# Optimization experiments

Measured on AMD Instinct MI355X. Metric: run time of the kernel, lower is better.

## Reference

```python
import jax, jax.numpy as jnp
import numpy as np

MIN_POS = 1e-6
EPS = 1e-20
B, S, F_IN, E, H = 2, 1024, 768, 768, 12
DH = E // H   # nnmf in_features per head (64)
FH = E // H   # nnmf out_features per head (hidden_features=embed_dim default)
N_NNMF_ITERS = 3
N_ALPHA_ITERS = 3


def l1norm(x, axis=-1):
    # F.normalize(x, p=1, dim=axis, eps=1e-20) for non-negative x
    return x / jnp.maximum(jnp.sum(jnp.abs(x), axis=axis, keepdims=True), EPS)


def setup_inputs() -> dict:
    key = jax.random.key(0)
    k = jax.random.split(key, 6)
    return {
        "x": jax.random.normal(k[0], (B, S, F_IN), jnp.float32),
        "embed_w": jax.random.normal(k[1], (E, F_IN), jnp.float32) * 0.02,
        "embed_b": jnp.zeros((E,), jnp.float32),
        "nnmf_w": jax.random.uniform(k[2], (FH, DH), jnp.float32),  # non-negative NMF dictionary
        "out_w": jax.random.normal(k[3], (F_IN, E), jnp.float32) * 0.02,
        "out_b": jnp.zeros((F_IN,), jnp.float32),
    }


def reference(x, embed_w, embed_b, nnmf_w, out_w, out_b):
    # normalize NMF weight rows (p=1 over in_features), as nnmf_layer.normalize_weights
    W = nnmf_w / jnp.maximum(jnp.sum(nnmf_w, axis=1, keepdims=True), EPS)  # [FH, DH]

    # embed + clamp positive, split heads
    xe = jnp.clip(x @ embed_w.T + embed_b, MIN_POS)            # [B,S,E]
    xe = xe.reshape(B, S, H, DH)                                # [B,S,H,DH]

    # NNMFDense: prepared_input = l1-normalized input (normalize_input_dim=-1)
    inp = l1norm(xe)                                            # [B,S,H,DH]
    h = l1norm(jnp.ones((B, S, H, FH), x.dtype))                # init hidden
    rec = inp
    for _ in range(N_NNMF_ITERS):
        rec = l1norm(jnp.clip(h @ W, MIN_POS))                  # reconstruction [B,S,H,DH]
        h = l1norm(jnp.clip(h * ((inp / rec) @ W.T), MIN_POS))  # multiplicative update

    # normalize_h (p=1, dim=-1)
    h = l1norm(h)                                               # [B,S,H,FH] -> 'bohf'

    # alpha dynamics fixed point
    alpha = jnp.ones((B, H, S, S), x.dtype)                     # 'bhoi'
    h_rec_input = rec * inp                                     # [B,S,H,DH]
    for _ in range(N_ALPHA_ITERS):
        h_mixed = jnp.einsum('bohf,bhoi->bihf', h, alpha)       # [B,S,H,FH]
        arec_inv = 1.0 / (h_mixed @ W + EPS)                    # _reconstruct -> [B,S,H,DH]
        alpha = alpha * jnp.einsum('bohf,bihf->bhoi', h_rec_input, arec_inv)

    out = jnp.einsum('bohf,bhoi->bihf', h, alpha)               # [B,S,H,FH]
    out = out.reshape(B, S, E)                                  # flatten heads
    return out @ out_w.T + out_b                                # out_project
```

## Files before the change

kernel.cpp:

```cpp
#include <hip/hip_runtime.h>

#define B_  2
#define S_  1024
#define FIN 768
#define E_  768
#define H_  12
#define DH  64

typedef unsigned int uint;
typedef unsigned short ushort;
typedef __attribute__((ext_vector_type(8))) short short8;
typedef __attribute__((ext_vector_type(4))) float floatx4;

__device__ __forceinline__ ushort f2bf(float f) {
    uint u = __float_as_uint(f);
    return (ushort)((u + 0x7fffu + ((u >> 16) & 1u)) >> 16);
}

__device__ __forceinline__ uint4 pack8(const ushort* p) {
    uint4 r;
    r.x = (uint)p[0] | ((uint)p[1] << 16);
    r.y = (uint)p[2] | ((uint)p[3] << 16);
    r.z = (uint)p[4] | ((uint)p[5] << 16);
    r.w = (uint)p[6] | ((uint)p[7] << 16);
    return r;
}

__device__ __forceinline__ void split8v(float4 a, float4 b, short8& hi, short8& lo) {
    float v[8] = {a.x, a.y, a.z, a.w, b.x, b.y, b.z, b.w};
    ushort h[8], l[8];
#pragma unroll
    for (int j = 0; j < 8; ++j) {
        h[j] = f2bf(v[j]);
        l[j] = f2bf(v[j] - __uint_as_float(((uint)h[j]) << 16));
    }
    uint4 H = pack8(h), L = pack8(l);
    hi = *(short8*)&H;
    lo = *(short8*)&L;
}

__global__ __launch_bounds__(256) void k_conv(const float* __restrict__ xs,
                                              const float* __restrict__ ew,
                                              const float* __restrict__ nw,
                                              ushort* __restrict__ xsH,
                                              ushort* __restrict__ xsL,
                                              ushort* __restrict__ ewH,
                                              ushort* __restrict__ ewL,
                                              float* __restrict__ Wn,
                                              float* __restrict__ r1inv,
                                              ushort* __restrict__ Wfrag) {
    __shared__ float Wl[64 * 65];
    const int tid = threadIdx.x, bid = blockIdx.x;

    if (bid < 768) {
        const size_t i = ((size_t)bid * 256 + tid) * 8;
        short8 hi, lo;
        split8v(*(const float4*)(xs + i), *(const float4*)(xs + i + 4), hi, lo);
        *(short8*)(xsH + i) = hi;
        *(short8*)(xsL + i) = lo;
        return;
    }
    if (bid < 1056) {
        const size_t i = ((size_t)(bid - 768) * 256 + tid) * 8;
        short8 hi, lo;
        split8v(*(const float4*)(ew + i), *(const float4*)(ew + i + 4), hi, lo);
        *(short8*)(ewH + i) = hi;
        *(short8*)(ewL + i) = lo;
        return;
    }

    const int f = tid >> 2, q = tid & 3;
    float v[16];
    float s = 0.f;
#pragma unroll
    for (int i = 0; i < 16; ++i) { v[i] = nw[f * 64 + q * 16 + i]; s += v[i]; }
    s += __shfl_xor(s, 1, 64);
    s += __shfl_xor(s, 2, 64);
    const float inv = 1.f / fmaxf(s, 1e-20f);
    float w[16];
#pragma unroll
    for (int i = 0; i < 16; ++i) {
        w[i] = v[i] * inv;
        Wn[f * 64 + q * 16 + i] = w[i];
        Wl[f * 65 + q * 16 + i] = w[i];
    }
    __syncthreads();
    if (tid < 64) {
        float cs = 0.f;
        for (int ff = 0; ff < 64; ++ff) cs += Wl[ff * 65 + tid];
        float t = fmaxf(cs * (1.f / 64.f), 1e-6f);
        float S = t;
#pragma unroll
        for (int m = 1; m < 64; m <<= 1) S += __shfl_xor(S, m, 64);
        S = fmaxf(S, 1e-20f);
        r1inv[tid] = S / t;
    }
    {
        short8 h0, l0, h1, l1;
        split8v(make_float4(w[0], w[1], w[2], w[3]),
                make_float4(w[4], w[5], w[6], w[7]), h0, l0);
        split8v(make_float4(w[8], w[9], w[10], w[11]),
                make_float4(w[12], w[13], w[14], w[15]), h1, l1);
        ushort* WwH = Wfrag + 2 * 4096;
        ushort* WwL = Wfrag + 3 * 4096;
        *(short8*)(WwH + f * 64 + q * 16) = h0;
        *(short8*)(WwH + f * 64 + q * 16 + 8) = h1;
        *(short8*)(WwL + f * 64 + q * 16) = l0;
        *(short8*)(WwL + f * 64 + q * 16 + 8) = l1;
    }
    {
        float t[16];
#pragma unroll
        for (int i = 0; i < 16; ++i) t[i] = Wl[(q * 16 + i) * 65 + f];
        short8 h0, l0, h1, l1;
        split8v(make_float4(t[0], t[1], t[2], t[3]),
                make_float4(t[4], t[5], t[6], t[7]), h0, l0);
        split8v(make_float4(t[8], t[9], t[10], t[11]),
                make_float4(t[12], t[13], t[14], t[15]), h1, l1);
        ushort* WtH = Wfrag;
        ushort* WtL = Wfrag + 4096;
        *(short8*)(WtH + f * 64 + q * 16) = h0;
        *(short8*)(WtH + f * 64 + q * 16 + 8) = h1;
        *(short8*)(WtL + f * 64 + q * 16) = l0;
        *(short8*)(WtL + f * 64 + q * 16 + 8) = l1;
    }
}

__device__ __forceinline__ void mfma_matvec(const float srcC[4][4], float* T,
                                            int lm, int lq,
                                            const ushort* WH, const ushort* WL,
                                            floatx4 out[4]) {
    __builtin_amdgcn_wave_barrier();
#pragma unroll
    for (int nt = 0; nt < 4; ++nt)
#pragma unroll
        for (int r = 0; r < 4; ++r)
            T[(lq * 4 + r) * 68 + nt * 16 + lm] = srcC[nt][r];
    __builtin_amdgcn_wave_barrier();
    float4 a00 = *(const float4*)&T[lm * 68 + lq * 8];
    float4 a01 = *(const float4*)&T[lm * 68 + lq * 8 + 4];
    float4 a10 = *(const float4*)&T[lm * 68 + 32 + lq * 8];
    float4 a11 = *(const float4*)&T[lm * 68 + 32 + lq * 8 + 4];
    __builtin_amdgcn_wave_barrier();
    short8 A0h, A0l, A1h, A1l;
    split8v(a00, a01, A0h, A0l);
    split8v(a10, a11, A1h, A1l);
#pragma unroll
    for (int nt = 0; nt < 4; ++nt) {
        const int row = (nt * 16 + lm) * 72;
        short8 b0h = *(const short8*)&WH[row + lq * 8];
        short8 b0l = *(const short8*)&WL[row + lq * 8];
        short8 b1h = *(const short8*)&WH[row + 32 + lq * 8];
        short8 b1l = *(const short8*)&WL[row + 32 + lq * 8];
        floatx4 acc0 = (floatx4)0.f, acc1 = (floatx4)0.f;
        acc0 = __builtin_amdgcn_mfma_f32_16x16x32_bf16(A0h, b0h, acc0, 0, 0, 0);
        acc0 = __builtin_amdgcn_mfma_f32_16x16x32_bf16(A0l, b0h, acc0, 0, 0, 0);
        acc0 = __builtin_amdgcn_mfma_f32_16x16x32_bf16(A0h, b0l, acc0, 0, 0, 0);
        acc1 = __builtin_amdgcn_mfma_f32_16x16x32_bf16(A1h, b1h, acc1, 0, 0, 0);
        acc1 = __builtin_amdgcn_mfma_f32_16x16x32_bf16(A1l, b1h, acc1, 0, 0, 0);
        acc1 = __builtin_amdgcn_mfma_f32_16x16x32_bf16(A1h, b1l, acc1, 0, 0, 0);
        out[nt] = acc0 + acc1;
    }
}

__global__ __launch_bounds__(256) void k_embed_nnmf(const ushort* __restrict__ xsH,
                                                    const ushort* __restrict__ xsL,
                                                    const ushort* __restrict__ ewH,
                                                    const ushort* __restrict__ ewL,
                                                    const float* __restrict__ eb,
                                                    const ushort* __restrict__ Wfrag,
                                                    const float* __restrict__ r1inv,
                                                    float* __restrict__ hout,
                                                    float* __restrict__ hriout,
                                                    float* __restrict__ mp0) {
    __shared__ __align__(16) unsigned char smem[73728];
    ushort* const sm = (ushort*)smem;
    const int tid = threadIdx.x;
    const int bid = blockIdx.x;

    const int head = bid % 12;
    const int tok0 = (bid / 12) * 64;

    const int wv = tid >> 6, lane = tid & 63;
    const int mbase = wv * 16;
    const int lm = lane & 15, lq = lane >> 4;

    floatx4 accA[4], accB[4];
#pragma unroll
    for (int nt = 0; nt < 4; ++nt) { accA[nt] = (floatx4)0.f; accB[nt] = (floatx4)0.f; }

    const int srow = tid >> 2, skq = (tid & 3) * 16;
    const int off = srow * 72 + skq;
    const ushort* xh = xsH + (size_t)(tok0 + srow) * FIN + skq;
    const ushort* xl = xsL + (size_t)(tok0 + srow) * FIN + skq;
    const ushort* wh = ewH + (size_t)(head * 64 + srow) * FIN + skq;
    const ushort* wl = ewL + (size_t)(head * 64 + srow) * FIN + skq;

    short8 pa[4], pb[4];
    pa[0] = *(const short8*)(xh);  pa[1] = *(const short8*)(xh + 8);
    pa[2] = *(const short8*)(xl);  pa[3] = *(const short8*)(xl + 8);
    pb[0] = *(const short8*)(wh);  pb[1] = *(const short8*)(wh + 8);
    pb[2] = *(const short8*)(wl);  pb[3] = *(const short8*)(wl + 8);
    {
        ushort* b0 = sm;
        *(short8*)&b0[off]            = pa[0];
        *(short8*)&b0[off + 8]        = pa[1];
        *(short8*)&b0[4608 + off]     = pa[2];
        *(short8*)&b0[4608 + off + 8] = pa[3];
        *(short8*)&b0[9216 + off]     = pb[0];
        *(short8*)&b0[9216 + off + 8] = pb[1];
        *(short8*)&b0[13824 + off]    = pb[2];
        *(short8*)&b0[13824 + off + 8]= pb[3];
    }
    pa[0] = *(const short8*)(xh + 64);  pa[1] = *(const short8*)(xh + 72);
    pa[2] = *(const short8*)(xl + 64);  pa[3] = *(const short8*)(xl + 72);
    pb[0] = *(const short8*)(wh + 64);  pb[1] = *(const short8*)(wh + 72);
    pb[2] = *(const short8*)(wl + 64);  pb[3] = *(const short8*)(wl + 72);
    __syncthreads();

#pragma unroll 2
    for (int kb = 0; kb < 12; ++kb) {
        const int cur = kb & 1;
        const ushort* cb = sm + cur * 18432;
#pragma unroll
        for (int ch = 0; ch < 2; ++ch) {
            const int ko = ch * 32 + lq * 8;
            short8 ah = *(const short8*)&cb[(mbase + lm) * 72 + ko];
            short8 al = *(const short8*)&cb[4608 + (mbase + lm) * 72 + ko];
#pragma unroll
            for (int nt = 0; nt < 4; ++nt) {
                short8 bh = *(const short8*)&cb[9216 + (nt * 16 + lm) * 72 + ko];
                short8 bl = *(const short8*)&cb[13824 + (nt * 16 + lm) * 72 + ko];
                accA[nt] = __builtin_amdgcn_mfma_f32_16x16x32_bf16(ah, bh, accA[nt], 0, 0, 0);
                accB[nt] = __builtin_amdgcn_mfma_f32_16x16x32_bf16(al, bh, accB[nt], 0, 0, 0);
                accB[nt] = __builtin_amdgcn_mfma_f32_16x16x32_bf16(ah, bl, accB[nt], 0, 0, 0);
            }
        }
        if (kb + 1 < 12) {
            ushort* sb = sm + (cur ^ 1) * 18432;
            *(short8*)&sb[off]            = pa[0];
            *(short8*)&sb[off + 8]        = pa[1];
            *(short8*)&sb[4608 + off]     = pa[2];
            *(short8*)&sb[4608 + off + 8] = pa[3];
            *(short8*)&sb[9216 + off]     = pb[0];
            *(short8*)&sb[9216 + off + 8] = pb[1];
            *(short8*)&sb[13824 + off]    = pb[2];
            *(short8*)&sb[13824 + off + 8]= pb[3];
        }
        if (kb + 2 < 12) {
            const int ko = (kb + 2) * 64;
            pa[0] = *(const short8*)(xh + ko);  pa[1] = *(const short8*)(xh + ko + 8);
            pa[2] = *(const short8*)(xl + ko);  pa[3] = *(const short8*)(xl + ko + 8);
            pb[0] = *(const short8*)(wh + ko);  pb[1] = *(const short8*)(wh + ko + 8);
            pb[2] = *(const short8*)(wl + ko);  pb[3] = *(const short8*)(wl + ko + 8);
        }
        __syncthreads();
    }

    const int wrow = tid >> 2, wkq = (tid & 3) * 16;
    const int wg = wrow * 64 + wkq;
    short8 wt0 = *(const short8*)(Wfrag + wg);
    short8 wt1 = *(const short8*)(Wfrag + wg + 8);
    short8 wt2 = *(const short8*)(Wfrag + 4096 + wg);
    short8 wt3 = *(const short8*)(Wfrag + 4096 + wg + 8);
    short8 ww0 = *(const short8*)(Wfrag + 8192 + wg);
    short8 ww1 = *(const short8*)(Wfrag + 8192 + wg + 8);
    short8 ww2 = *(const short8*)(Wfrag + 12288 + wg);
    short8 ww3 = *(const short8*)(Wfrag + 12288 + wg + 8);
    float r1c[4];
#pragma unroll
    for (int nt = 0; nt < 4; ++nt) r1c[nt] = r1inv[nt * 16 + lm];

    float inpC[4][4];
    {
        float bb[4];
#pragma unroll
        for (int nt = 0; nt < 4; ++nt) bb[nt] = eb[head * 64 + nt * 16 + lm];
#pragma unroll
        for (int r = 0; r < 4; ++r) {
            float e[4];
            float p = 0.f;
#pragma unroll
            for (int nt = 0; nt < 4; ++nt) {
                e[nt] = fmaxf((accA[nt][r] + accB[nt][r]) + bb[nt], 1e-6f);
                p += e[nt];
            }
            p += __shfl_xor(p, 1, 64);
            p += __shfl_xor(p, 2, 64);
            p += __shfl_xor(p, 4, 64);
            p += __shfl_xor(p, 8, 64);
            const float inv = 1.f / fmaxf(p, 1e-20f);
#pragma unroll
            for (int nt = 0; nt < 4; ++nt) inpC[nt][r] = e[nt] * inv;
        }
    }

    __syncthreads();
    ushort* WtH = sm;
    ushort* WtL = sm + 4608;
    ushort* WwH = sm + 9216;
    ushort* WwL = sm + 13824;
    float*  Tb  = (float*)(smem + 36864);
    float*  pbuf= (float*)(smem + 54272);
    float*  T   = Tb + wv * (16 * 68);
    {
        const int l = wrow * 72 + wkq;
        *(short8*)&WtH[l]     = wt0;
        *(short8*)&WtH[l + 8] = wt1;
        *(short8*)&WtL[l]     = wt2;
        *(short8*)&WtL[l + 8] = wt3;
        *(short8*)&WwH[l]     = ww0;
        *(short8*)&WwH[l + 8] = ww1;
        *(short8*)&WwL[l]     = ww2;
        *(short8*)&WwL[l + 8] = ww3;
    }
    __syncthreads();

    const size_t obase = ((size_t)((tok0 >> 10) * 12 + head) * 1024 + (tok0 & 1023));
    const size_t rowbase = obase + wv * 16;

    float hC[4][4], recC[4][4];
    {
        float qC[4][4];
#pragma unroll
        for (int nt = 0; nt < 4; ++nt)
#pragma unroll
            for (int r = 0; r < 4; ++r) qC[nt][r] = inpC[nt][r] * r1c[nt];
        floatx4 u[4];
        mfma_matvec(qC, T, lm, lq, WwH, WwL, u);
#pragma unroll
        for (int nt = 0; nt < 4; ++nt)
#pragma unroll
            for (int r = 0; r < 4; ++r)
                hC[nt][r] = fmaxf(u[nt][r] * (1.f / 64.f), 1e-6f);
#pragma unroll
        for (int r = 0; r < 4; ++r) {
            float s = (hC[0][r] + hC[1][r]) + (hC[2][r] + hC[3][r]);
            s += __shfl_xor(s, 1, 64); s += __shfl_xor(s, 2, 64);
            s += __shfl_xor(s, 4, 64); s += __shfl_xor(s, 8, 64);
            const float inv = __builtin_amdgcn_rcpf(fmaxf(s, 1e-20f));
#pragma unroll
            for (int nt = 0; nt < 4; ++nt) hC[nt][r] *= inv;
        }
    }
#pragma unroll 1
    for (int it = 0; it < 2; ++it) {
        floatx4 t[4];
        mfma_matvec(hC, T, lm, lq, WtH, WtL, t);
        float tC[4][4], qC[4][4];
#pragma unroll
        for (int nt = 0; nt < 4; ++nt)
#pragma unroll
            for (int r = 0; r < 4; ++r) tC[nt][r] = fmaxf(t[nt][r], 1e-6f);
#pragma unroll
        for (int r = 0; r < 4; ++r) {
            float s = (tC[0][r] + tC[1][r]) + (tC[2][r] + tC[3][r]);
            s += __shfl_xor(s, 1, 64); s += __shfl_xor(s, 2, 64);
            s += __shfl_xor(s, 4, 64); s += __shfl_xor(s, 8, 64);
            s = fmaxf(s, 1e-20f);
            const float invS = __builtin_amdgcn_rcpf(s);
#pragma unroll
            for (int nt = 0; nt < 4; ++nt) {
                recC[nt][r] = tC[nt][r] * invS;
                qC[nt][r] = inpC[nt][r] * s * __builtin_amdgcn_rcpf(tC[nt][r]);
            }
        }
        floatx4 u[4];
        mfma_matvec(qC, T, lm, lq, WwH, WwL, u);
#pragma unroll
        for (int nt = 0; nt < 4; ++nt)
#pragma unroll
            for (int r = 0; r < 4; ++r)
                hC[nt][r] = fmaxf(hC[nt][r] * u[nt][r], 1e-6f);
#pragma unroll
        for (int r = 0; r < 4; ++r) {
            float s = (hC[0][r] + hC[1][r]) + (hC[2][r] + hC[3][r]);
            s += __shfl_xor(s, 1, 64); s += __shfl_xor(s, 2, 64);
            s += __shfl_xor(s, 4, 64); s += __shfl_xor(s, 8, 64);
            const float inv = __builtin_amdgcn_rcpf(fmaxf(s, 1e-20f));
#pragma unroll
            for (int nt = 0; nt < 4; ++nt) hC[nt][r] *= inv;
        }
    }
#pragma unroll
    for (int r = 0; r < 4; ++r) {
        float s = (hC[0][r] + hC[1][r]) + (hC[2][r] + hC[3][r]);
        s += __shfl_xor(s, 1, 64); s += __shfl_xor(s, 2, 64);
        s += __shfl_xor(s, 4, 64); s += __shfl_xor(s, 8, 64);
        const float inv = __builtin_amdgcn_rcpf(fmaxf(s, 1e-20f));
#pragma unroll
        for (int nt = 0; nt < 4; ++nt) hC[nt][r] *= inv;
    }

#pragma unroll
    for (int nt = 0; nt < 4; ++nt)
#pragma unroll
        for (int r = 0; r < 4; ++r) {
            const size_t o = (rowbase + lq * 4 + r) * 64 + nt * 16 + lm;
            hout[o] = hC[nt][r];
            hriout[o] = recC[nt][r] * inpC[nt][r];
        }

    float hs[4];
#pragma unroll
    for (int nt = 0; nt < 4; ++nt) {
        float s = (hC[nt][0] + hC[nt][1]) + (hC[nt][2] + hC[nt][3]);
        s += __shfl_xor(s, 16, 64);
        s += __shfl_xor(s, 32, 64);
        hs[nt] = s;
    }
    pbuf[wv * 64 + lq * 16 + lm] = hs[lq];
    __syncthreads();
    if (tid < 64) {
        float tot = (pbuf[tid] + pbuf[64 + tid]) + (pbuf[128 + tid] + pbuf[192 + tid]);
        mp0[(obase >> 6) * 64 + tid] = tot;
    }
}

__global__ __launch_bounds__(256) void k_alpha_step(const float* __restrict__ hin,
                                                    const float* __restrict__ hri,
                                                    const float* __restrict__ Wn,
                                                    const float* __restrict__ mp_in,
                                                    float* __restrict__ mp_out,
                                                    float* __restrict__ c,
                                                    int it) {
    __shared__ float mred[4][64];
    __shared__ float mv[64];
    __shared__ float vv[64];
    __shared__ float cl[64];
    const int tid = threadIdx.x;
    const int bh = blockIdx.x >> 4;
    const int chunk = blockIdx.x & 15;
    const size_t rowbase = (size_t)bh * 1024 + chunk * 64;

    {
        int f = tid & 63, p = tid >> 6;
        float s = 0.f;
#pragma unroll
        for (int pp = 0; pp < 4; ++pp)
            s += mp_in[((size_t)bh * 16 + p * 4 + pp) * 64 + f];
        mred[p][f] = s;
    }
    __syncthreads();
    if (tid < 64)
        mv[tid] = (mred[0][tid] + mred[1][tid]) + (mred[2][tid] + mred[3][tid]);
    __syncthreads();
    {
        int d = tid & 63, qq = tid >> 6;
        float r = 0.f;
#pragma unroll
        for (int ff = 0; ff < 16; ++ff)
            r = fmaf(mv[qq * 16 + ff], Wn[(size_t)(qq * 16 + ff) * 64 + d], r);
        mred[qq][d] = r;
    }
    __syncthreads();
    if (tid < 64)
        vv[tid] = 1.f / (((mred[0][tid] + mred[1][tid]) + (mred[2][tid] + mred[3][tid])) + 1e-20f);
    __syncthreads();
    {
        int o = tid >> 2, dq = tid & 3;
        const float* rp = hri + (rowbase + o) * 64 + dq * 16;
        float dot = 0.f;
#pragma unroll
        for (int t4 = 0; t4 < 16; t4 += 4) {
            float4 r4 = *(const float4*)(rp + t4);
            dot = fmaf(r4.x, vv[dq * 16 + t4 + 0], dot);
            dot = fmaf(r4.y, vv[dq * 16 + t4 + 1], dot);
            dot = fmaf(r4.z, vv[dq * 16 + t4 + 2], dot);
            dot = fmaf(r4.w, vv[dq * 16 + t4 + 3], dot);
        }
        dot += __shfl_xor(dot, 1, 64);
        dot += __shfl_xor(dot, 2, 64);
        float cn = dot;
        if (it >= 2) cn *= c[rowbase + o];
        if (dq == 0) { c[rowbase + o] = cn; cl[o] = cn; }
    }
    __syncthreads();
    {
        const int f4 = (tid & 15) * 4, ogr = tid >> 4;
        float4 a = make_float4(0.f, 0.f, 0.f, 0.f);
#pragma unroll
        for (int oi = 0; oi < 4; ++oi) {
            int o = ogr * 4 + oi;
            float4 h4 = *(const float4*)(hin + (rowbase + o) * 64 + f4);
            float cv = cl[o];
            a.x = fmaf(h4.x, cv, a.x); a.y = fmaf(h4.y, cv, a.y);
            a.z = fmaf(h4.z, cv, a.z); a.w = fmaf(h4.w, cv, a.w);
        }
        a.x += __shfl_xor(a.x, 16, 64); a.y += __shfl_xor(a.y, 16, 64);
        a.z += __shfl_xor(a.z, 16, 64); a.w += __shfl_xor(a.w, 16, 64);
        a.x += __shfl_xor(a.x, 32, 64); a.y += __shfl_xor(a.y, 32, 64);
        a.z += __shfl_xor(a.z, 32, 64); a.w += __shfl_xor(a.w, 32, 64);
        const int w = tid >> 6;
        if ((tid & 63) < 16) *(float4*)&mred[w][(tid & 15) * 4] = a;
    }
    __syncthreads();
    if (tid < 64) {
        float s = (mred[0][tid] + mred[1][tid]) + (mred[2][tid] + mred[3][tid]);
        mp_out[((size_t)bh * 16 + chunk) * 64 + tid] = s;
    }
}

__global__ __launch_bounds__(256) void k_projbcast(const float* __restrict__ mp3,
                                                   const float* __restrict__ ow,
                                                   const float* __restrict__ ob,
                                                   float* __restrict__ out) {
    __shared__ float Ml[768];
    __shared__ float ps[4][64];
    __shared__ float yseg[64];
    const int tid = threadIdx.x;
    const int b = blockIdx.x / 192;
    const int rem = blockIdx.x - b * 192;
    const int jt = rem >> 4, rg = rem & 15;
    for (int i = tid; i < 768; i += 256) {
        const int hh = i >> 6, f = i & 63;
        const float* src = mp3 + ((size_t)(b * 12 + hh) * 16) * 64 + f;
        float s = 0.f;
#pragma unroll
        for (int cc = 0; cc < 16; ++cc) s += src[cc * 64];
        Ml[i] = s;
    }
    __syncthreads();
    const int jj = tid & 63, part = tid >> 6;
    const int j = jt * 64 + jj;
    const float* row = ow + (size_t)j * 768 + part * 192;
    float acc = 0.f;
    for (int t = 0; t < 192; t += 4) {
        float4 w4 = *(const float4*)(row + t);
        acc = fmaf(w4.x, Ml[part * 192 + t + 0], acc);
        acc = fmaf(w4.y, Ml[part * 192 + t + 1], acc);
        acc = fmaf(w4.z, Ml[part * 192 + t + 2], acc);
        acc = fmaf(w4.w, Ml[part * 192 + t + 3], acc);
    }
    ps[part][jj] = acc;
    __syncthreads();
    if (tid < 64)
        yseg[tid] = ps[0][tid] + ps[1][tid] + ps[2][tid] + ps[3][tid] + ob[jt * 64 + tid];
    __syncthreads();
    const int r0 = tid >> 2, c4 = (tid & 3) * 16;
    float4 v4[4];
#pragma unroll
    for (int q = 0; q < 4; ++q) v4[q] = *(const float4*)&yseg[c4 + q * 4];
    float* dst = out + ((size_t)(b * 1024 + rg * 64 + r0)) * 768 + jt * 64 + c4;
#pragma unroll
    for (int q = 0; q < 4; ++q) *(float4*)(dst + q * 4) = v4[q];
}

extern "C" void kernel_launch(void* const* d_in, const int* in_sizes, int n_in,
                              void* d_out, int out_size, void* d_ws, size_t ws_size,
                              hipStream_t stream) {
    const float* xs = (const float*)d_in[0];
    const float* ew = (const float*)d_in[1];
    const float* eb = (const float*)d_in[2];
    const float* nw = (const float*)d_in[3];
    const float* ow = (const float*)d_in[4];
    const float* ob = (const float*)d_in[5];
    float* out = (float*)d_out;

    float* ws    = (float*)d_ws;
    float* h     = ws + 1572864;
    float* hri   = ws + 3145728;
    float* Wn    = ws + 4718592;
    float* r1inv = ws + 4722688;
    float* mp0   = ws + 4722944;
    float* mp1   = ws + 4747520;
    float* mp2   = ws + 4772096;
    float* c     = ws + 4796672;
    ushort* xsH  = (ushort*)(ws + 4821248);
    ushort* xsL  = (ushort*)(ws + 5607680);
    ushort* ewH  = (ushort*)(ws + 6394112);
    ushort* ewL  = (ushort*)(ws + 6689024);
    ushort* Wfrag= (ushort*)(ws + 6983936);

    k_conv<<<1057, 256, 0, stream>>>(xs, ew, nw, xsH, xsL, ewH, ewL, Wn, r1inv, Wfrag);
    k_embed_nnmf<<<384, 256, 0, stream>>>(xsH, xsL, ewH, ewL, eb, Wfrag, r1inv, h, hri, mp0);
    k_alpha_step<<<384, 256, 0, stream>>>(h, hri, Wn, mp0, mp1, c, 1);
    k_alpha_step<<<384, 256, 0, stream>>>(h, hri, Wn, mp1, mp2, c, 2);
    k_alpha_step<<<384, 256, 0, stream>>>(h, hri, Wn, mp2, mp1, c, 3);
    k_projbcast<<<384, 256, 0, stream>>>(mp1, ow, ob, out);
}
```

Baseline: 128.3 us.

## Fold bf16 split conversion and NMF weight prep into consumer kernels

Drops the separate conversion kernel that split x, embed_w and the NMF dictionary into bf16 hi/lo arrays. The embed kernel now loads fp32 tiles and does the hi/lo split before staging them in shared memory, and it normalizes and transposes the NMF weights itself. The alpha-step kernels recompute the normalized dictionary into shared memory. This removes one launch and a write-then-read of the converted arrays through global memory, at the cost of fp32 loads moving twice the bytes in the GEMM loop and of redundant weight preparation in every block.

Measured after the change: 131.8 us. +2.8%, slower.

```diff
diff --git a/kernel.cpp b/kernel.cpp
--- a/kernel.cpp
+++ b/kernel.cpp
@@ -37,93 +37,6 @@
     uint4 H = pack8(h), L = pack8(l);
     hi = *(short8*)&H;
     lo = *(short8*)&L;
-}
-
-__global__ __launch_bounds__(256) void k_conv(const float* __restrict__ xs,
-                                              const float* __restrict__ ew,
-                                              const float* __restrict__ nw,
-                                              ushort* __restrict__ xsH,
-                                              ushort* __restrict__ xsL,
-                                              ushort* __restrict__ ewH,
-                                              ushort* __restrict__ ewL,
-                                              float* __restrict__ Wn,
-                                              float* __restrict__ r1inv,
-                                              ushort* __restrict__ Wfrag) {
-    __shared__ float Wl[64 * 65];
-    const int tid = threadIdx.x, bid = blockIdx.x;
-
-    if (bid < 768) {
-        const size_t i = ((size_t)bid * 256 + tid) * 8;
-        short8 hi, lo;
-        split8v(*(const float4*)(xs + i), *(const float4*)(xs + i + 4), hi, lo);
-        *(short8*)(xsH + i) = hi;
-        *(short8*)(xsL + i) = lo;
-        return;
-    }
-    if (bid < 1056) {
-        const size_t i = ((size_t)(bid - 768) * 256 + tid) * 8;
-        short8 hi, lo;
-        split8v(*(const float4*)(ew + i), *(const float4*)(ew + i + 4), hi, lo);
-        *(short8*)(ewH + i) = hi;
-        *(short8*)(ewL + i) = lo;
-        return;
-    }
-
-    const int f = tid >> 2, q = tid & 3;
-    float v[16];
-    float s = 0.f;
-#pragma unroll
-    for (int i = 0; i < 16; ++i) { v[i] = nw[f * 64 + q * 16 + i]; s += v[i]; }
-    s += __shfl_xor(s, 1, 64);
-    s += __shfl_xor(s, 2, 64);
-    const float inv = 1.f / fmaxf(s, 1e-20f);
-    float w[16];
-#pragma unroll
-    for (int i = 0; i < 16; ++i) {
-        w[i] = v[i] * inv;
-        Wn[f * 64 + q * 16 + i] = w[i];
-        Wl[f * 65 + q * 16 + i] = w[i];
-    }
-    __syncthreads();
-    if (tid < 64) {
-        float cs = 0.f;
-        for (int ff = 0; ff < 64; ++ff) cs += Wl[ff * 65 + tid];
-        float t = fmaxf(cs * (1.f / 64.f), 1e-6f);
-        float S = t;
-#pragma unroll
-        for (int m = 1; m < 64; m <<= 1) S += __shfl_xor(S, m, 64);
-        S = fmaxf(S, 1e-20f);
-        r1inv[tid] = S / t;
-    }
-    {
-        short8 h0, l0, h1, l1;
-        split8v(make_float4(w[0], w[1], w[2], w[3]),
-                make_float4(w[4], w[5], w[6], w[7]), h0, l0);
-        split8v(make_float4(w[8], w[9], w[10], w[11]),
-                make_float4(w[12], w[13], w[14], w[15]), h1, l1);
-        ushort* WwH = Wfrag + 2 * 4096;
-        ushort* WwL = Wfrag + 3 * 4096;
-        *(short8*)(WwH + f * 64 + q * 16) = h0;
-        *(short8*)(WwH + f * 64 + q * 16 + 8) = h1;
-        *(short8*)(WwL + f * 64 + q * 16) = l0;
-        *(short8*)(WwL + f * 64 + q * 16 + 8) = l1;
-    }
-    {
-        float t[16];
-#pragma unroll
-        for (int i = 0; i < 16; ++i) t[i] = Wl[(q * 16 + i) * 65 + f];
-        short8 h0, l0, h1, l1;
-        split8v(make_float4(t[0], t[1], t[2], t[3]),
-                make_float4(t[4], t[5], t[6], t[7]), h0, l0);
-        split8v(make_float4(t[8], t[9], t[10], t[11]),
-                make_float4(t[12], t[13], t[14], t[15]), h1, l1);
-        ushort* WtH = Wfrag;
-        ushort* WtL = Wfrag + 4096;
-        *(short8*)(WtH + f * 64 + q * 16) = h0;
-        *(short8*)(WtH + f * 64 + q * 16 + 8) = h1;
-        *(short8*)(WtL + f * 64 + q * 16) = l0;
-        *(short8*)(WtL + f * 64 + q * 16 + 8) = l1;
-    }
 }
 
 __device__ __forceinline__ void mfma_matvec(const float srcC[4][4], float* T,
@@ -163,13 +76,10 @@
     }
 }
 
-__global__ __launch_bounds__(256) void k_embed_nnmf(const ushort* __restrict__ xsH,
-                                                    const ushort* __restrict__ xsL,
-                                                    const ushort* __restrict__ ewH,
-                                                    const ushort* __restrict__ ewL,
+__global__ __launch_bounds__(256) void k_embed_nnmf(const float* __restrict__ xs,
+                                                    const float* __restrict__ ew,
                                                     const float* __restrict__ eb,
-                                                    const ushort* __restrict__ Wfrag,
-                                                    const float* __restrict__ r1inv,
+                                                    const float* __restrict__ nw,
                                                     float* __restrict__ hout,
                                                     float* __restrict__ hriout,
                                                     float* __restrict__ mp0) {
@@ -191,31 +101,34 @@
 
     const int srow = tid >> 2, skq = (tid & 3) * 16;
     const int off = srow * 72 + skq;
-    const ushort* xh = xsH + (size_t)(tok0 + srow) * FIN + skq;
-    const ushort* xl = xsL + (size_t)(tok0 + srow) * FIN + skq;
-    const ushort* wh = ewH + (size_t)(head * 64 + srow) * FIN + skq;
-    const ushort* wl = ewL + (size_t)(head * 64 + srow) * FIN + skq;
-
-    short8 pa[4], pb[4];
-    pa[0] = *(const short8*)(xh);  pa[1] = *(const short8*)(xh + 8);
-    pa[2] = *(const short8*)(xl);  pa[3] = *(const short8*)(xl + 8);
-    pb[0] = *(const short8*)(wh);  pb[1] = *(const short8*)(wh + 8);
-    pb[2] = *(const short8*)(wl);  pb[3] = *(const short8*)(wl + 8);
+    const float* xrow = xs + (size_t)(tok0 + srow) * FIN + skq;
+    const float* wrow = ew + (size_t)(head * 64 + srow) * FIN + skq;
+
+    float4 qa[4], qb[4];
+#pragma unroll
+    for (int c = 0; c < 4; ++c) {
+        qa[c] = *(const float4*)(xrow + c * 4);
+        qb[c] = *(const float4*)(wrow + c * 4);
+    }
     {
         ushort* b0 = sm;
-        *(short8*)&b0[off]            = pa[0];
-        *(short8*)&b0[off + 8]        = pa[1];
-        *(short8*)&b0[4608 + off]     = pa[2];
-        *(short8*)&b0[4608 + off + 8] = pa[3];
-        *(short8*)&b0[9216 + off]     = pb[0];
-        *(short8*)&b0[9216 + off + 8] = pb[1];
-        *(short8*)&b0[13824 + off]    = pb[2];
-        *(short8*)&b0[13824 + off + 8]= pb[3];
-    }
-    pa[0] = *(const short8*)(xh + 64);  pa[1] = *(const short8*)(xh + 72);
-    pa[2] = *(const short8*)(xl + 64);  pa[3] = *(const short8*)(xl + 72);
-    pb[0] = *(const short8*)(wh + 64);  pb[1] = *(const short8*)(wh + 72);
-    pb[2] = *(const short8*)(wl + 64);  pb[3] = *(const short8*)(wl + 72);
+        short8 h0, l0, h1, l1;
+        split8v(qa[0], qa[1], h0, l0); split8v(qa[2], qa[3], h1, l1);
+        *(short8*)&b0[off]            = h0;
+        *(short8*)&b0[off + 8]        = h1;
+        *(short8*)&b0[4608 + off]     = l0;
+        *(short8*)&b0[4608 + off + 8] = l1;
+        split8v(qb[0], qb[1], h0, l0); split8v(qb[2], qb[3], h1, l1);
+        *(short8*)&b0[9216 + off]     = h0;
+        *(short8*)&b0[9216 + off + 8] = h1;
+        *(short8*)&b0[13824 + off]    = l0;
+        *(short8*)&b0[13824 + off + 8]= l1;
+    }
+#pragma unroll
+    for (int c = 0; c < 4; ++c) {
+        qa[c] = *(const float4*)(xrow + 64 + c * 4);
+        qb[c] = *(const float4*)(wrow + 64 + c * 4);
+    }
     __syncthreads();
 
 #pragma unroll 2
@@ -238,38 +151,28 @@
         }
         if (kb + 1 < 12) {
             ushort* sb = sm + (cur ^ 1) * 18432;
-            *(short8*)&sb[off]            = pa[0];
-            *(short8*)&sb[off + 8]        = pa[1];
-            *(short8*)&sb[4608 + off]     = pa[2];
-            *(short8*)&sb[4608 + off + 8] = pa[3];
-            *(short8*)&sb[9216 + off]     = pb[0];
-            *(short8*)&sb[9216 + off + 8] = pb[1];
-            *(short8*)&sb[13824 + off]    = pb[2];
-            *(short8*)&sb[13824 + off + 8]= pb[3];
+            short8 h0, l0, h1, l1;
+            split8v(qa[0], qa[1], h0, l0); split8v(qa[2], qa[3], h1, l1);
+            *(short8*)&sb[off]            = h0;
+            *(short8*)&sb[off + 8]        = h1;
+            *(short8*)&sb[4608 + off]     = l0;
+            *(short8*)&sb[4608 + off + 8] = l1;
+            split8v(qb[0], qb[1], h0, l0); split8v(qb[2], qb[3], h1, l1);
+            *(short8*)&sb[9216 + off]     = h0;
+            *(short8*)&sb[9216 + off + 8] = h1;
+            *(short8*)&sb[13824 + off]    = l0;
+            *(short8*)&sb[13824 + off + 8]= l1;
         }
         if (kb + 2 < 12) {
             const int ko = (kb + 2) * 64;
-            pa[0] = *(const short8*)(xh + ko);  pa[1] = *(const short8*)(xh + ko + 8);
-            pa[2] = *(const short8*)(xl + ko);  pa[3] = *(const short8*)(xl + ko + 8);
-            pb[0] = *(const short8*)(wh + ko);  pb[1] = *(const short8*)(wh + ko + 8);
-            pb[2] = *(const short8*)(wl + ko);  pb[3] = *(const short8*)(wl + ko + 8);
+#pragma unroll
+            for (int c = 0; c < 4; ++c) {
+                qa[c] = *(const float4*)(xrow + ko + c * 4);
+                qb[c] = *(const float4*)(wrow + ko + c * 4);
+            }
         }
         __syncthreads();
     }
-
-    const int wrow = tid >> 2, wkq = (tid & 3) * 16;
-    const int wg = wrow * 64 + wkq;
-    short8 wt0 = *(const short8*)(Wfrag + wg);
-    short8 wt1 = *(const short8*)(Wfrag + wg + 8);
-    short8 wt2 = *(const short8*)(Wfrag + 4096 + wg);
-    short8 wt3 = *(const short8*)(Wfrag + 4096 + wg + 8);
-    short8 ww0 = *(const short8*)(Wfrag + 8192 + wg);
-    short8 ww1 = *(const short8*)(Wfrag + 8192 + wg + 8);
-    short8 ww2 = *(const short8*)(Wfrag + 12288 + wg);
-    short8 ww3 = *(const short8*)(Wfrag + 12288 + wg + 8);
-    float r1c[4];
-#pragma unroll
-    for (int nt = 0; nt < 4; ++nt) r1c[nt] = r1inv[nt * 16 + lm];
 
     float inpC[4][4];
     {
@@ -300,21 +203,64 @@
     ushort* WtL = sm + 4608;
     ushort* WwH = sm + 9216;
     ushort* WwL = sm + 13824;
-    float*  Tb  = (float*)(smem + 36864);
-    float*  pbuf= (float*)(smem + 54272);
+    float*  Wl  = (float*)(smem + 36864);
+    float*  Tb  = (float*)(smem + 53504);
+    float*  pbuf= (float*)(smem + 70912);
     float*  T   = Tb + wv * (16 * 68);
-    {
-        const int l = wrow * 72 + wkq;
-        *(short8*)&WtH[l]     = wt0;
-        *(short8*)&WtH[l + 8] = wt1;
-        *(short8*)&WtL[l]     = wt2;
-        *(short8*)&WtL[l + 8] = wt3;
-        *(short8*)&WwH[l]     = ww0;
-        *(short8*)&WwH[l + 8] = ww1;
-        *(short8*)&WwL[l]     = ww2;
-        *(short8*)&WwL[l + 8] = ww3;
-    }
-    __syncthreads();
+
+    const int pf = tid >> 2, pq = tid & 3;
+    {
+        float v[16];
+        float s = 0.f;
+#pragma unroll
+        for (int i = 0; i < 16; ++i) { v[i] = nw[pf * 64 + pq * 16 + i]; s += v[i]; }
+        s += __shfl_xor(s, 1, 64);
+        s += __shfl_xor(s, 2, 64);
+        const float inv = 1.f / fmaxf(s, 1e-20f);
+        float w[16];
+#pragma unroll
+        for (int i = 0; i < 16; ++i) { w[i] = v[i] * inv; Wl[pf * 65 + pq * 16 + i] = w[i]; }
+        short8 h0, l0, h1, l1;
+        split8v(make_float4(w[0], w[1], w[2], w[3]),
+                make_float4(w[4], w[5], w[6], w[7]), h0, l0);
+        split8v(make_float4(w[8], w[9], w[10], w[11]),
+                make_float4(w[12], w[13], w[14], w[15]), h1, l1);
+        const int l = pf * 72 + pq * 16;
+        *(short8*)&WwH[l]     = h0;
+        *(short8*)&WwH[l + 8] = h1;
+        *(short8*)&WwL[l]     = l0;
+        *(short8*)&WwL[l + 8] = l1;
+    }
+    __syncthreads();
+    {
+        float t[16];
+#pragma unroll
+        for (int i = 0; i < 16; ++i) t[i] = Wl[(pq * 16 + i) * 65 + pf];
+        short8 h0, l0, h1, l1;
+        split8v(make_float4(t[0], t[1], t[2], t[3]),
+                make_float4(t[4], t[5], t[6], t[7]), h0, l0);
+        split8v(make_float4(t[8], t[9], t[10], t[11]),
+                make_float4(t[12], t[13], t[14], t[15]), h1, l1);
+        const int l = pf * 72 + pq * 16;
+        *(short8*)&WtH[l]     = h0;
+        *(short8*)&WtH[l + 8] = h1;
+        *(short8*)&WtL[l]     = l0;
+        *(short8*)&WtL[l + 8] = l1;
+    }
+    if (tid < 64) {
+        float cs = 0.f;
+        for (int ff = 0; ff < 64; ++ff) cs += Wl[ff * 65 + tid];
+        float t = fmaxf(cs * (1.f / 64.f), 1e-6f);
+        float S = t;
+#pragma unroll
+        for (int m = 1; m < 64; m <<= 1) S += __shfl_xor(S, m, 64);
+        S = fmaxf(S, 1e-20f);
+        pbuf[tid] = S / t;
+    }
+    __syncthreads();
+    float r1c[4];
+#pragma unroll
+    for (int nt = 0; nt < 4; ++nt) r1c[nt] = pbuf[nt * 16 + lm];
 
     const size_t obase = ((size_t)((tok0 >> 10) * 12 + head) * 1024 + (tok0 & 1023));
     const size_t rowbase = obase + wv * 16;
@@ -409,6 +355,7 @@
         s += __shfl_xor(s, 32, 64);
         hs[nt] = s;
     }
+    __syncthreads();
     pbuf[wv * 64 + lq * 16 + lm] = hs[lq];
     __syncthreads();
     if (tid < 64) {
@@ -419,11 +366,12 @@
 
 __global__ __launch_bounds__(256) void k_alpha_step(const float* __restrict__ hin,
                                                     const float* __restrict__ hri,
-                                                    const float* __restrict__ Wn,
+                                                    const float* __restrict__ nw,
                                                     const float* __restrict__ mp_in,
                                                     float* __restrict__ mp_out,
                                                     float* __restrict__ c,
                                                     int it) {
+    __shared__ float Wnl[64 * 65];
     __shared__ float mred[4][64];
     __shared__ float mv[64];
     __shared__ float vv[64];
@@ -434,6 +382,18 @@
     const size_t rowbase = (size_t)bh * 1024 + chunk * 64;
 
     {
+        const int pf = tid >> 2, pq = tid & 3;
+        float v[16];
+        float s = 0.f;
+#pragma unroll
+        for (int i = 0; i < 16; ++i) { v[i] = nw[pf * 64 + pq * 16 + i]; s += v[i]; }
+        s += __shfl_xor(s, 1, 64);
+        s += __shfl_xor(s, 2, 64);
+        const float inv = 1.f / fmaxf(s, 1e-20f);
+#pragma unroll
+        for (int i = 0; i < 16; ++i) Wnl[pf * 65 + pq * 16 + i] = v[i] * inv;
+    }
+    {
         int f = tid & 63, p = tid >> 6;
         float s = 0.f;
 #pragma unroll
@@ -450,7 +410,7 @@
         float r = 0.f;
 #pragma unroll
         for (int ff = 0; ff < 16; ++ff)
-            r = fmaf(mv[qq * 16 + ff], Wn[(size_t)(qq * 16 + ff) * 64 + d], r);
+            r = fmaf(mv[qq * 16 + ff], Wnl[(qq * 16 + ff) * 65 + d], r);
         mred[qq][d] = r;
     }
     __syncthreads();
@@ -557,25 +517,17 @@
     const float* ob = (const float*)d_in[5];
     float* out = (float*)d_out;
 
-    float* ws    = (float*)d_ws;
-    float* h     = ws + 1572864;
-    float* hri   = ws + 3145728;
-    float* Wn    = ws + 4718592;
-    float* r1inv = ws + 4722688;
-    float* mp0   = ws + 4722944;
-    float* mp1   = ws + 4747520;
-    float* mp2   = ws + 4772096;
-    float* c     = ws + 4796672;
-    ushort* xsH  = (ushort*)(ws + 4821248);
-    ushort* xsL  = (ushort*)(ws + 5607680);
-    ushort* ewH  = (ushort*)(ws + 6394112);
-    ushort* ewL  = (ushort*)(ws + 6689024);
-    ushort* Wfrag= (ushort*)(ws + 6983936);
-
-    k_conv<<<1057, 256, 0, stream>>>(xs, ew, nw, xsH, xsL, ewH, ewL, Wn, r1inv, Wfrag);
-    k_embed_nnmf<<<384, 256, 0, stream>>>(xsH, xsL, ewH, ewL, eb, Wfrag, r1inv, h, hri, mp0);
-    k_alpha_step<<<384, 256, 0, stream>>>(h, hri, Wn, mp0, mp1, c, 1);
-    k_alpha_step<<<384, 256, 0, stream>>>(h, hri, Wn, mp1, mp2, c, 2);
-    k_alpha_step<<<384, 256, 0, stream>>>(h, hri, Wn, mp2, mp1, c, 3);
+    float* ws  = (float*)d_ws;
+    float* h   = ws;
+    float* hri = ws + 1572864;
+    float* mp0 = ws + 3145728;
+    float* mp1 = ws + 3170304;
+    float* mp2 = ws + 3194880;
+    float* c   = ws + 3219456;
+
+    k_embed_nnmf<<<384, 256, 0, stream>>>(xs, ew, eb, nw, h, hri, mp0);
+    k_alpha_step<<<384, 256, 0, stream>>>(h, hri, nw, mp0, mp1, c, 1);
+    k_alpha_step<<<384, 256, 0, stream>>>(h, hri, nw, mp1, mp2, c, 2);
+    k_alpha_step<<<384, 256, 0, stream>>>(h, hri, nw, mp2, mp1, c, 3);
     k_projbcast<<<384, 256, 0, stream>>>(mp1, ow, ob, out);
 }
```
